# Kernel optimization log

Measured on AMD Instinct MI355X. Metric: run time of the kernel, lower is better.

The kernel has to match this reference:

```python
import jax, jax.numpy as jnp
import numpy as np

N_NODES = 100000
N_EDGES = 3200000

def setup_inputs() -> dict:
    key = jax.random.key(0)
    ks = jax.random.split(key, 8)
    x = jax.random.normal(ks[0], (N_NODES, 22), dtype=jnp.float32)
    edge_index = jax.random.randint(ks[1], (2, N_EDGES), 0, N_NODES, dtype=jnp.int64)
    W1 = jax.random.normal(ks[2], (22, 64), dtype=jnp.float32) * 0.1
    b1 = jnp.zeros((64,), dtype=jnp.float32)
    W2 = jax.random.normal(ks[3], (64, 64), dtype=jnp.float32) * 0.1
    b2 = jnp.zeros((64,), dtype=jnp.float32)
    Wf = jax.random.normal(ks[4], (64, 1), dtype=jnp.float32) * 0.1
    bf = jnp.zeros((1,), dtype=jnp.float32)
    return {"x": x, "edge_index": edge_index, "W1": W1, "b1": b1,
            "W2": W2, "b2": b2, "Wf": Wf, "bf": bf}

def _prep_graph(edge_index, n):
    # PyG GCNConv default: add self-loops, symmetric normalization
    loops = jnp.arange(n, dtype=edge_index.dtype)
    src = jnp.concatenate([edge_index[0], loops])
    dst = jnp.concatenate([edge_index[1], loops])
    deg = jnp.zeros((n,), jnp.float32).at[dst].add(1.0)  # in-degree incl. self-loop
    dinv = jax.lax.rsqrt(deg)
    norm = dinv[src] * dinv[dst]  # [E+N]
    return src, dst, norm

def _gcn_conv(h, W, b, src, dst, norm, n):
    h = h @ W                               # [N, F_out] transform first (F_out small)
    msg = h[src] * norm[:, None]            # gather + scale, [E+N, F_out]
    agg = jax.ops.segment_sum(msg, dst, num_segments=n)  # scatter-add
    return agg + b

def reference(x, edge_index, W1, b1, W2, b2, Wf, bf):
    n = x.shape[0]
    src, dst, norm = _prep_graph(edge_index, n)
    h = jax.nn.relu(_gcn_conv(x, W1, b1, src, dst, norm, n))
    # dropout is identity in eval mode
    h = jax.nn.relu(_gcn_conv(h, W2, b2, src, dst, norm, n))
    return h @ Wf + bf
```

## Files before the change

kernel.cpp:

```cpp
#include <hip/hip_runtime.h>
#include <hip/hip_fp16.h>
#include <stdint.h>


static constexpr int FIN = 22;
static constexpr int NWIN = 8;
static constexpr int XW = 16;

struct H8 { __half2 h[4]; };

__global__ void k_zero(int* cnt, int N) {
  int i = blockIdx.x * blockDim.x + threadIdx.x;
  int stride = gridDim.x * blockDim.x;
  for (; i < N; i += stride) cnt[i] = 0;
}

__global__ void k_detect(const unsigned int* w, int E, int* flag) {
  int t = threadIdx.x;
  size_t pos = 2ull * ((size_t)t * (size_t)(E / 64)) + 1ull;
  unsigned v = w[pos];
  unsigned long long b = __ballot(v != 0u);
  if (t == 0) *flag = (b == 0ull) ? 1 : 0;
}

__device__ __forceinline__ int load_idx(const void* ei, size_t i, int is64) {
  return is64 ? (int)((const long long*)ei)[i] : ((const int*)ei)[i];
}

__global__ void k_count(const void* ei, const int* __restrict__ flag, int* cnt,
                        int* src32, int* dst32, int E) {
  int is64 = *flag;
  int i = blockIdx.x * blockDim.x + threadIdx.x;
  int stride = gridDim.x * blockDim.x;
  for (; i < E; i += stride) {
    int s = load_idx(ei, (size_t)i, is64);
    int d = load_idx(ei, (size_t)E + (size_t)i, is64);
    src32[i] = s;
    dst32[i] = d;
    atomicAdd(&cnt[d], 1);
  }
}

__global__ void k_scan1(const int* __restrict__ cnt, int* partial, int N) {
  __shared__ int sh[256];
  int b = blockIdx.x, t = threadIdx.x;
  int i0 = b * 1024 + t * 4;
  int s = 0;
#pragma unroll
  for (int k = 0; k < 4; ++k) {
    int i = i0 + k;
    if (i < N) s += cnt[i];
  }
  sh[t] = s;
  __syncthreads();
  for (int off = 128; off > 0; off >>= 1) {
    if (t < off) sh[t] += sh[t + off];
    __syncthreads();
  }
  if (t == 0) partial[b] = sh[0];
}

__global__ void k_scan2(int* partial, int nb) {
  __shared__ int sh[128];
  int t = threadIdx.x;
  int v = (t < nb) ? partial[t] : 0;
  sh[t] = v;
  __syncthreads();
  for (int off = 1; off < 128; off <<= 1) {
    int u = (t >= off) ? sh[t - off] : 0;
    __syncthreads();
    sh[t] += u;
    __syncthreads();
  }
  if (t < nb) partial[t] = sh[t] - v;
}

__global__ void k_scan3(const int* __restrict__ cnt, const int* __restrict__ base,
                        int* row_ptr, int* fillc, float* dinv, int N) {
  __shared__ int sh[256];
  int b = blockIdx.x, t = threadIdx.x;
  int i0 = b * 1024 + t * 4;
  int c[4];
  int s = 0;
#pragma unroll
  for (int k = 0; k < 4; ++k) {
    int i = i0 + k;
    c[k] = (i < N) ? cnt[i] : 0;
    s += c[k];
  }
  sh[t] = s;
  __syncthreads();
  int v = s;
  for (int off = 1; off < 256; off <<= 1) {
    int u = (t >= off) ? sh[t - off] : 0;
    __syncthreads();
    sh[t] += u;
    __syncthreads();
  }
  int excl = sh[t] - v + base[b];
#pragma unroll
  for (int k = 0; k < 4; ++k) {
    int i = i0 + k;
    if (i < N) {
      row_ptr[i] = excl;
      fillc[i] = excl;
      dinv[i] = rsqrtf((float)(c[k] + 1));
      excl += c[k];
    }
  }
  if (b == gridDim.x - 1 && t == 255) row_ptr[N] = excl;
}

__global__ void k_fill_win(const int* __restrict__ src32, const int* __restrict__ dst32,
                           int* fillc, int* colv, int E, int winsize) {
  int win = blockIdx.x % NWIN;
  int lo = win * winsize, hi = lo + winsize;
  int nb = gridDim.x / NWIN;
  int bw = blockIdx.x / NWIN;
  long long i = (long long)bw * blockDim.x + threadIdx.x;
  long long stride = (long long)nb * blockDim.x;
  for (; i < E; i += stride) {
    int d = dst32[i];
    if (d >= lo && d < hi) {
      int s = src32[i];
      int p = atomicAdd(&fillc[d], 1);
      colv[p] = s;
    }
  }
}

__global__ void k_xs(const float* __restrict__ x, const float* __restrict__ dinv,
                     __half2* __restrict__ xs2, int N) {
  int i = blockIdx.x * blockDim.x + threadIdx.x;
  int stride = gridDim.x * blockDim.x;
  int total = N * XW;
  for (; i < total; i += stride) {
    int node = i >> 4, w = i & (XW - 1);
    float a = 0.f, b = 0.f;
    if (2 * w < FIN) {
      float di = dinv[node];
      a = x[(size_t)node * FIN + 2 * w] * di;
      b = x[(size_t)node * FIN + 2 * w + 1] * di;
    }
    xs2[i] = __floats2half2_rn(a, b);
  }
}

__global__ void k_agg1(const H8* __restrict__ xs4, const int* __restrict__ row_ptr,
                       const int* __restrict__ colv, const float* __restrict__ dinv,
                       const float* __restrict__ W1, const float* __restrict__ b1,
                       __half* __restrict__ s2h, int N) {
  __shared__ float w1[FIN * 64];
  int t = threadIdx.x;
  for (int i = t; i < FIN * 64; i += blockDim.x) w1[i] = W1[i];
  __syncthreads();
  int wib = t >> 6, lane = t & 63;
  int node = blockIdx.x * 4 + wib;
  if (node >= N) return;
  int eslot = lane >> 2, fg = lane & 3;
  int start = row_ptr[node], end = row_ptr[node + 1];
  float ax[4] = {0.f, 0.f, 0.f, 0.f}, ay[4] = {0.f, 0.f, 0.f, 0.f};
  for (int pos = start; pos < end; pos += 64) {
#pragma unroll
    for (int g = 0; g < 4; ++g) {
      int e = pos + g * 16 + eslot;
      int a = colv[min(e, end - 1)];
      H8 v = xs4[(size_t)a * 4 + fg];
      float msk = (e < end) ? 1.f : 0.f;
#pragma unroll
      for (int w = 0; w < 4; ++w) {
        float2 f = __half22float2(v.h[w]);
        ax[w] += msk * f.x;
        ay[w] += msk * f.y;
      }
    }
  }
#pragma unroll
  for (int m = 4; m <= 32; m <<= 1) {
#pragma unroll
    for (int w = 0; w < 4; ++w) {
      ax[w] += __shfl_xor(ax[w], m);
      ay[w] += __shfl_xor(ay[w], m);
    }
  }
  float di = dinv[node];
  H8 sv = xs4[(size_t)node * 4 + fg];
  float tt[8];
#pragma unroll
  for (int w = 0; w < 4; ++w) {
    float2 f = __half22float2(sv.h[w]);
    tt[2 * w]     = di * (ax[w] + f.x);
    tt[2 * w + 1] = di * (ay[w] + f.y);
  }
  float o = 0.f;
#pragma unroll
  for (int k = 0; k < FIN; ++k) {
    float tk = __shfl(tt[k & 7], k >> 3);
    o += tk * w1[k * 64 + lane];
  }
  float h = fmaxf(o + b1[lane], 0.f);
  s2h[(size_t)node * 64 + lane] = __float2half(h * di);
}

__global__ void k_agg2(const H8* __restrict__ s2q, const int* __restrict__ row_ptr,
                       const int* __restrict__ colv, const float* __restrict__ dinv,
                       const float* __restrict__ W2, const float* __restrict__ b2,
                       const float* __restrict__ Wf, const float* __restrict__ bf,
                       float* __restrict__ out, int N) {
  __shared__ float w2[64 * 64];
  int t = threadIdx.x;
  for (int i = t; i < 64 * 64; i += blockDim.x) w2[i] = W2[i];
  __syncthreads();
  int wib = t >> 6, lane = t & 63;
  int node = blockIdx.x * 4 + wib;
  if (node >= N) return;
  int eslot = lane >> 3, fg = lane & 7;
  int start = row_ptr[node], end = row_ptr[node + 1];
  float ax[4] = {0.f, 0.f, 0.f, 0.f}, ay[4] = {0.f, 0.f, 0.f, 0.f};
  for (int pos = start; pos < end; pos += 32) {
#pragma unroll
    for (int g = 0; g < 4; ++g) {
      int e = pos + g * 8 + eslot;
      int a = colv[min(e, end - 1)];
      H8 v = s2q[(size_t)a * 8 + fg];
      float msk = (e < end) ? 1.f : 0.f;
#pragma unroll
      for (int w = 0; w < 4; ++w) {
        float2 f = __half22float2(v.h[w]);
        ax[w] += msk * f.x;
        ay[w] += msk * f.y;
      }
    }
  }
#pragma unroll
  for (int m = 8; m <= 32; m <<= 1) {
#pragma unroll
    for (int w = 0; w < 4; ++w) {
      ax[w] += __shfl_xor(ax[w], m);
      ay[w] += __shfl_xor(ay[w], m);
    }
  }
  float di = dinv[node];
  H8 sv = s2q[(size_t)node * 8 + fg];
  float tt[8];
#pragma unroll
  for (int w = 0; w < 4; ++w) {
    float2 f = __half22float2(sv.h[w]);
    tt[2 * w]     = di * (ax[w] + f.x);
    tt[2 * w + 1] = di * (ay[w] + f.y);
  }
  float o = 0.f;
#pragma unroll
  for (int k = 0; k < 64; ++k) {
    float tk = __shfl(tt[k & 7], k >> 3);
    o += tk * w2[k * 64 + lane];
  }
  float h = fmaxf(o + b2[lane], 0.f);
  float v = h * Wf[lane];
#pragma unroll
  for (int off = 32; off > 0; off >>= 1) v += __shfl_down(v, off);
  if (lane == 0) out[node] = v + bf[0];
}

extern "C" void kernel_launch(void* const* d_in, const int* in_sizes, int n_in,
                              void* d_out, int out_size, void* d_ws, size_t ws_size,
                              hipStream_t stream) {
  const float* x  = (const float*)d_in[0];
  const void*  ei = d_in[1];
  const float* W1 = (const float*)d_in[2];
  const float* b1 = (const float*)d_in[3];
  const float* W2 = (const float*)d_in[4];
  const float* b2 = (const float*)d_in[5];
  const float* Wf = (const float*)d_in[6];
  const float* bf = (const float*)d_in[7];
  int N = in_sizes[0] / FIN;
  int E = in_sizes[1] / 2;
  float* outp = (float*)d_out;

  char* p = (char*)d_ws;
  auto alloc = [&](size_t bytes) {
    void* r = (void*)p;
    p += (bytes + 255) & ~(size_t)255;
    return r;
  };
  int*     cnt     = (int*)alloc((size_t)N * 4);
  int*     row_ptr = (int*)alloc(((size_t)N + 1) * 4);
  int*     fillc   = (int*)alloc((size_t)N * 4);
  float*   dinv    = (float*)alloc((size_t)N * 4);
  int*     flag    = (int*)alloc(256);
  int*     partial = (int*)alloc(1024);
  int*     colv    = (int*)alloc((size_t)E * 4);
  int*     src32   = (int*)alloc((size_t)E * 4);
  int*     dst32   = (int*)alloc((size_t)E * 4);
  __half2* xs2     = (__half2*)alloc((size_t)N * XW * 4);
  __half*  s2h     = (__half*)alloc((size_t)N * 64 * 2);
  (void)ws_size; (void)n_in; (void)out_size;

  int egrid = min((E + 255) / 256, 12544);
  int ngrid = (N + 255) / 256;
  int sgrid = (N + 1023) / 1024;
  int xgrid = min((N * XW + 255) / 256, 8704);
  int wgrid = (N + 3) / 4;
  int winsize = (N + NWIN - 1) / NWIN;

  k_zero    <<<ngrid, 256, 0, stream>>>(cnt, N);
  k_detect  <<<1, 64, 0, stream>>>((const unsigned int*)ei, E, flag);
  k_count   <<<egrid, 256, 0, stream>>>(ei, flag, cnt, src32, dst32, E);
  k_scan1   <<<sgrid, 256, 0, stream>>>(cnt, partial, N);
  k_scan2   <<<1, 128, 0, stream>>>(partial, sgrid);
  k_scan3   <<<sgrid, 256, 0, stream>>>(cnt, partial, row_ptr, fillc, dinv, N);
  k_fill_win<<<2048, 256, 0, stream>>>(src32, dst32, fillc, colv, E, winsize);
  k_xs      <<<xgrid, 256, 0, stream>>>(x, dinv, xs2, N);
  k_agg1    <<<wgrid, 256, 0, stream>>>((const H8*)xs2, row_ptr, colv, dinv, W1, b1, s2h, N);
  k_agg2    <<<wgrid, 256, 0, stream>>>((const H8*)s2h, row_ptr, colv, dinv,
                                        W2, b2, Wf, bf, outp, N);
}
```

Before: 596.2 us.

## Store layer-1 features as scaled FP8 and gather edge indices via wave shuffles

The intermediate layer-1 activations are now quantized to FP8 e4m3 with a fixed scale of 16 instead of fp16, which halves the bytes gathered per edge in the second aggregation. The lane mapping is reworked so each lane loads 16 bytes (16 features) per edge and decodes them with hardware FP8 conversions. The first aggregation loads a block of 64 column indices once per wave and broadcasts them with shuffles instead of redundant per-lane loads. Nontemporal loads are added for streaming index arrays. FP8 precision with a fixed scale risks accuracy loss or saturation on inputs with different value ranges.

Measured after the change: 628.5 us. 1.05x slower.

```diff
diff --git a/kernel.cpp b/kernel.cpp
--- a/kernel.cpp
+++ b/kernel.cpp
@@ -1,13 +1,26 @@
 #include <hip/hip_runtime.h>
 #include <hip/hip_fp16.h>
+#include <hip/hip_fp8.h>
 #include <stdint.h>
 
 
 static constexpr int FIN = 22;
 static constexpr int NWIN = 8;
 static constexpr int XW = 16;
+static constexpr float S2SCALE = 16.f;
 
 struct H8 { __half2 h[4]; };
+
+template <int SEL>
+__device__ __forceinline__ float fp8_to_f32(unsigned w) {
+#if __has_builtin(__builtin_amdgcn_cvt_f32_fp8)
+  return __builtin_amdgcn_cvt_f32_fp8((int)w, SEL);
+#else
+  __hip_fp8_e4m3 t;
+  t.__x = (__hip_fp8_storage_t)((w >> (8 * SEL)) & 0xffu);
+  return (float)t;
+#endif
+}
 
 __global__ void k_zero(int* cnt, int N) {
   int i = blockIdx.x * blockDim.x + threadIdx.x;
@@ -120,7 +133,7 @@
   long long i = (long long)bw * blockDim.x + threadIdx.x;
   long long stride = (long long)nb * blockDim.x;
   for (; i < E; i += stride) {
-    int d = dst32[i];
+    int d = __builtin_nontemporal_load(dst32 + i);
     if (d >= lo && d < hi) {
       int s = src32[i];
       int p = atomicAdd(&fillc[d], 1);
@@ -149,7 +162,7 @@
 __global__ void k_agg1(const H8* __restrict__ xs4, const int* __restrict__ row_ptr,
                        const int* __restrict__ colv, const float* __restrict__ dinv,
                        const float* __restrict__ W1, const float* __restrict__ b1,
-                       __half* __restrict__ s2h, int N) {
+                       unsigned char* __restrict__ s2b, int N) {
   __shared__ float w1[FIN * 64];
   int t = threadIdx.x;
   for (int i = t; i < FIN * 64; i += blockDim.x) w1[i] = W1[i];
@@ -161,12 +174,14 @@
   int start = row_ptr[node], end = row_ptr[node + 1];
   float ax[4] = {0.f, 0.f, 0.f, 0.f}, ay[4] = {0.f, 0.f, 0.f, 0.f};
   for (int pos = start; pos < end; pos += 64) {
+    int m = end - pos;
+    int idx = (lane < m) ? __builtin_nontemporal_load(colv + pos + lane) : 0;
 #pragma unroll
     for (int g = 0; g < 4; ++g) {
-      int e = pos + g * 16 + eslot;
-      int a = colv[min(e, end - 1)];
+      int eoff = g * 16 + eslot;
+      int a = __shfl(idx, min(eoff, m - 1));
       H8 v = xs4[(size_t)a * 4 + fg];
-      float msk = (e < end) ? 1.f : 0.f;
+      float msk = (eoff < m) ? 1.f : 0.f;
 #pragma unroll
       for (int w = 0; w < 4; ++w) {
         float2 f = __half22float2(v.h[w]);
@@ -176,11 +191,11 @@
     }
   }
 #pragma unroll
-  for (int m = 4; m <= 32; m <<= 1) {
+  for (int m2 = 4; m2 <= 32; m2 <<= 1) {
 #pragma unroll
     for (int w = 0; w < 4; ++w) {
-      ax[w] += __shfl_xor(ax[w], m);
-      ay[w] += __shfl_xor(ay[w], m);
+      ax[w] += __shfl_xor(ax[w], m2);
+      ay[w] += __shfl_xor(ay[w], m2);
     }
   }
   float di = dinv[node];
@@ -199,10 +214,11 @@
     o += tk * w1[k * 64 + lane];
   }
   float h = fmaxf(o + b1[lane], 0.f);
-  s2h[(size_t)node * 64 + lane] = __float2half(h * di);
-}
-
-__global__ void k_agg2(const H8* __restrict__ s2q, const int* __restrict__ row_ptr,
+  __hip_fp8_e4m3 q(h * di * S2SCALE);
+  s2b[(size_t)node * 64 + lane] = (unsigned char)q.__x;
+}
+
+__global__ void k_agg2(const unsigned char* __restrict__ s2b, const int* __restrict__ row_ptr,
                        const int* __restrict__ colv, const float* __restrict__ dinv,
                        const float* __restrict__ W2, const float* __restrict__ b2,
                        const float* __restrict__ Wf, const float* __restrict__ bf,
@@ -214,45 +230,49 @@
   int wib = t >> 6, lane = t & 63;
   int node = blockIdx.x * 4 + wib;
   if (node >= N) return;
-  int eslot = lane >> 3, fg = lane & 7;
+  int eslot = lane >> 2, fg = lane & 3;
   int start = row_ptr[node], end = row_ptr[node + 1];
-  float ax[4] = {0.f, 0.f, 0.f, 0.f}, ay[4] = {0.f, 0.f, 0.f, 0.f};
+  float acc[16];
+#pragma unroll
+  for (int j = 0; j < 16; ++j) acc[j] = 0.f;
   for (int pos = start; pos < end; pos += 32) {
 #pragma unroll
-    for (int g = 0; g < 4; ++g) {
-      int e = pos + g * 8 + eslot;
-      int a = colv[min(e, end - 1)];
-      H8 v = s2q[(size_t)a * 8 + fg];
+    for (int g = 0; g < 2; ++g) {
+      int e = pos + g * 16 + eslot;
+      int a = __builtin_nontemporal_load(colv + min(e, end - 1));
+      uint4 v = *reinterpret_cast<const uint4*>(s2b + (size_t)a * 64 + fg * 16);
       float msk = (e < end) ? 1.f : 0.f;
 #pragma unroll
       for (int w = 0; w < 4; ++w) {
-        float2 f = __half22float2(v.h[w]);
-        ax[w] += msk * f.x;
-        ay[w] += msk * f.y;
+        unsigned wd = (w == 0) ? v.x : (w == 1) ? v.y : (w == 2) ? v.z : v.w;
+        acc[4 * w + 0] += msk * fp8_to_f32<0>(wd);
+        acc[4 * w + 1] += msk * fp8_to_f32<1>(wd);
+        acc[4 * w + 2] += msk * fp8_to_f32<2>(wd);
+        acc[4 * w + 3] += msk * fp8_to_f32<3>(wd);
       }
     }
   }
 #pragma unroll
-  for (int m = 8; m <= 32; m <<= 1) {
-#pragma unroll
-    for (int w = 0; w < 4; ++w) {
-      ax[w] += __shfl_xor(ax[w], m);
-      ay[w] += __shfl_xor(ay[w], m);
-    }
+  for (int m = 4; m <= 32; m <<= 1) {
+#pragma unroll
+    for (int j = 0; j < 16; ++j) acc[j] += __shfl_xor(acc[j], m);
   }
   float di = dinv[node];
-  H8 sv = s2q[(size_t)node * 8 + fg];
-  float tt[8];
+  float mul = di * (1.f / S2SCALE);
+  uint4 sv = *reinterpret_cast<const uint4*>(s2b + (size_t)node * 64 + fg * 16);
+  float tt[16];
 #pragma unroll
   for (int w = 0; w < 4; ++w) {
-    float2 f = __half22float2(sv.h[w]);
-    tt[2 * w]     = di * (ax[w] + f.x);
-    tt[2 * w + 1] = di * (ay[w] + f.y);
+    unsigned wd = (w == 0) ? sv.x : (w == 1) ? sv.y : (w == 2) ? sv.z : sv.w;
+    tt[4 * w + 0] = mul * (acc[4 * w + 0] + fp8_to_f32<0>(wd));
+    tt[4 * w + 1] = mul * (acc[4 * w + 1] + fp8_to_f32<1>(wd));
+    tt[4 * w + 2] = mul * (acc[4 * w + 2] + fp8_to_f32<2>(wd));
+    tt[4 * w + 3] = mul * (acc[4 * w + 3] + fp8_to_f32<3>(wd));
   }
   float o = 0.f;
 #pragma unroll
   for (int k = 0; k < 64; ++k) {
-    float tk = __shfl(tt[k & 7], k >> 3);
+    float tk = __shfl(tt[k & 15], k >> 4);
     o += tk * w2[k * 64 + lane];
   }
   float h = fmaxf(o + b2[lane], 0.f);
@@ -283,17 +303,17 @@
     p += (bytes + 255) & ~(size_t)255;
     return r;
   };
-  int*     cnt     = (int*)alloc((size_t)N * 4);
-  int*     row_ptr = (int*)alloc(((size_t)N + 1) * 4);
-  int*     fillc   = (int*)alloc((size_t)N * 4);
-  float*   dinv    = (float*)alloc((size_t)N * 4);
-  int*     flag    = (int*)alloc(256);
-  int*     partial = (int*)alloc(1024);
-  int*     colv    = (int*)alloc((size_t)E * 4);
-  int*     src32   = (int*)alloc((size_t)E * 4);
-  int*     dst32   = (int*)alloc((size_t)E * 4);
-  __half2* xs2     = (__half2*)alloc((size_t)N * XW * 4);
-  __half*  s2h     = (__half*)alloc((size_t)N * 64 * 2);
+  int*           cnt     = (int*)alloc((size_t)N * 4);
+  int*           row_ptr = (int*)alloc(((size_t)N + 1) * 4);
+  int*           fillc   = (int*)alloc((size_t)N * 4);
+  float*         dinv    = (float*)alloc((size_t)N * 4);
+  int*           flag    = (int*)alloc(256);
+  int*           partial = (int*)alloc(1024);
+  int*           colv    = (int*)alloc((size_t)E * 4);
+  int*           src32   = (int*)alloc((size_t)E * 4);
+  int*           dst32   = (int*)alloc((size_t)E * 4);
+  __half2*       xs2     = (__half2*)alloc((size_t)N * XW * 4);
+  unsigned char* s2b     = (unsigned char*)alloc((size_t)N * 64);
   (void)ws_size; (void)n_in; (void)out_size;
 
   int egrid = min((E + 255) / 256, 12544);
@@ -311,7 +331,7 @@
   k_scan3   <<<sgrid, 256, 0, stream>>>(cnt, partial, row_ptr, fillc, dinv, N);
   k_fill_win<<<2048, 256, 0, stream>>>(src32, dst32, fillc, colv, E, winsize);
   k_xs      <<<xgrid, 256, 0, stream>>>(x, dinv, xs2, N);
-  k_agg1    <<<wgrid, 256, 0, stream>>>((const H8*)xs2, row_ptr, colv, dinv, W1, b1, s2h, N);
-  k_agg2    <<<wgrid, 256, 0, stream>>>((const H8*)s2h, row_ptr, colv, dinv,
+  k_agg1    <<<wgrid, 256, 0, stream>>>((const H8*)xs2, row_ptr, colv, dinv, W1, b1, s2b, N);
+  k_agg2    <<<wgrid, 256, 0, stream>>>(s2b, row_ptr, colv, dinv,
                                         W2, b2, Wf, bf, outp, N);
 }
```
